# Kernel optimization log

Hardware: AMD Instinct MI355X
Metric: run time of the kernel (lower is better)

Reference implementation:

```python
import jax, jax.numpy as jnp
import numpy as np

D = 128  # embedding dimension (init arg d)

def setup_inputs() -> dict:
    key = jax.random.key(0)
    x = jax.random.uniform(key, (256, 4096), dtype=jnp.float32)  # (b, n) in [0,1]
    return {"x": x}

def reference(x) -> jnp.ndarray:
    # Fourier basis: emb[b, n, i] = cos(pi * i * x[b, n]), i = 0..D-1
    i = jnp.arange(D, dtype=x.dtype)  # (D,)
    emb = jnp.cos(jnp.pi * x[..., None] * i)  # (b, n, D)
    return emb
```

## Files before the change

### kernel.cpp

```cpp
#include <hip/hip_runtime.h>


typedef float f32x4 __attribute__((ext_vector_type(4)));

__global__ __launch_bounds__(256) void Emb_37967510896970_kernel(
    const float* __restrict__ x, f32x4* __restrict__ out, int total_rows)
{
    const int tid  = threadIdx.x;
    const int ty   = tid >> 5;
    const int slot = tid & 31;
    const int row0 = blockIdx.x * 64 + ty;

    float h[8];
#pragma unroll
    for (int q = 0; q < 8; ++q) {
        int r = row0 + 8 * q;
        h[q] = 0.5f * x[r < total_rows ? r : 0];
    }

    const float i0 = (float)(slot << 2);

    f32x4 v[8];
#pragma unroll
    for (int q = 0; q < 8; ++q) {
        const float hb = h[q] * i0;
#pragma unroll
        for (int k = 0; k < 4; ++k) {
            float ang = fmaf(h[q], (float)k, hb);
            v[q][k] = __builtin_amdgcn_cosf(__builtin_amdgcn_fractf(ang));
        }
    }

    f32x4* p = out + (size_t)blockIdx.x * 2048 + tid;
#pragma unroll
    for (int q = 0; q < 8; ++q) {
        int r = row0 + 8 * q;
        if (r < total_rows) __builtin_nontemporal_store(v[q], p + q * 256);
    }
}

extern "C" void kernel_launch(void* const* d_in, const int* in_sizes, int n_in,
                              void* d_out, int out_size, void* d_ws, size_t ws_size,
                              hipStream_t stream) {
    const float* x = (const float*)d_in[0];
    f32x4* out = (f32x4*)d_out;
    const int total_rows = in_sizes[0];
    const int grid = (total_rows + 63) / 64;
    Emb_37967510896970_kernel<<<grid, 256, 0, stream>>>(x, out, total_rows);
}
```

Baseline: 104.0 us.

## Use persistent grid-stride loop with prefetch of next rows' inputs

Replaces the one-block-per-64-rows launch with a fixed grid of 2048 blocks that loop over rows in grid strides. Each iteration prefetches the x values for the next stride before computing and storing the current one. The aim is to cut block scheduling overhead and hide the input load latency. In exchange, each thread carries extra registers, and a fixed grid may underfill or unbalance the device for other sizes.

```diff
diff --git a/kernel.cpp b/kernel.cpp
--- a/kernel.cpp
+++ b/kernel.cpp
@@ -9,33 +9,46 @@
     const int tid  = threadIdx.x;
     const int ty   = tid >> 5;
     const int slot = tid & 31;
-    const int row0 = blockIdx.x * 64 + ty;
+    const float i0 = (float)(slot << 2);
+    const int stride_rows = (int)gridDim.x * 64;
+
+    int base = blockIdx.x * 64;
 
     float h[8];
 #pragma unroll
     for (int q = 0; q < 8; ++q) {
-        int r = row0 + 8 * q;
+        int r = base + ty + 8 * q;
         h[q] = 0.5f * x[r < total_rows ? r : 0];
     }
 
-    const float i0 = (float)(slot << 2);
+    for (; base < total_rows; base += stride_rows) {
+        const int nb = base + stride_rows;
+        float hn[8];
+        if (nb < total_rows) {
+#pragma unroll
+            for (int q = 0; q < 8; ++q) {
+                int r = nb + ty + 8 * q;
+                hn[q] = 0.5f * x[r < total_rows ? r : 0];
+            }
+        }
 
-    f32x4 v[8];
+        f32x4* p = out + (size_t)base * 32 + tid;
 #pragma unroll
-    for (int q = 0; q < 8; ++q) {
-        const float hb = h[q] * i0;
+        for (int q = 0; q < 8; ++q) {
+            const float hq = h[q];
+            const float hb = hq * i0;
+            f32x4 v;
 #pragma unroll
-        for (int k = 0; k < 4; ++k) {
-            float ang = fmaf(h[q], (float)k, hb);
-            v[q][k] = __builtin_amdgcn_cosf(__builtin_amdgcn_fractf(ang));
+            for (int k = 0; k < 4; ++k)
+                v[k] = __builtin_amdgcn_cosf(
+                           __builtin_amdgcn_fractf(fmaf(hq, (float)k, hb)));
+            int r = base + ty + 8 * q;
+            if (r < total_rows)
+                __builtin_nontemporal_store(v, p + q * 256);
         }
-    }
 
-    f32x4* p = out + (size_t)blockIdx.x * 2048 + tid;
 #pragma unroll
-    for (int q = 0; q < 8; ++q) {
-        int r = row0 + 8 * q;
-        if (r < total_rows) __builtin_nontemporal_store(v[q], p + q * 256);
+        for (int q = 0; q < 8; ++q) h[q] = hn[q];
     }
 }
 
@@ -45,6 +58,6 @@
     const float* x = (const float*)d_in[0];
     f32x4* out = (f32x4*)d_out;
     const int total_rows = in_sizes[0];
-    const int grid = (total_rows + 63) / 64;
+    const int grid = 2048;
     Emb_37967510896970_kernel<<<grid, 256, 0, stream>>>(x, out, total_rows);
 }
```

After: 106.7 us. +2.6%, slower.

## Switch to persistent grid-stride kernel with prefetched input rows

Applied to the files above, without the earlier changes.

Replaces the one-block-per-64-rows launch with a fixed grid of 512 blocks that each sweep over rows with a grid stride. Each iteration computes and stores one 8-row by 128-column tile, and the x value two sweeps ahead is prefetched into a register rotation. The intent is to cut block launch overhead and keep stores streaming continuously. In exchange, each thread has less independent work in flight per iteration, and the persistent grid may underfill the GPU's compute units.

```diff
diff --git a/kernel.cpp b/kernel.cpp
--- a/kernel.cpp
+++ b/kernel.cpp
@@ -4,38 +4,41 @@
 typedef float f32x4 __attribute__((ext_vector_type(4)));
 
 __global__ __launch_bounds__(256) void Emb_37967510896970_kernel(
-    const float* __restrict__ x, f32x4* __restrict__ out, int total_rows)
+    const float* __restrict__ x, f32x4* __restrict__ out,
+    int total_rows, int nsweeps)
 {
     const int tid  = threadIdx.x;
     const int ty   = tid >> 5;
     const int slot = tid & 31;
-    const int row0 = blockIdx.x * 64 + ty;
-
-    float h[8];
-#pragma unroll
-    for (int q = 0; q < 8; ++q) {
-        int r = row0 + 8 * q;
-        h[q] = 0.5f * x[r < total_rows ? r : 0];
-    }
-
     const float i0 = (float)(slot << 2);
 
-    f32x4 v[8];
+    const int rstep = (int)gridDim.x * 8;
+    int row = blockIdx.x * 8 + ty;
+
+    float h0 = 0.5f * x[row < total_rows ? row : 0];
+    int r1 = row + rstep;
+    float h1 = 0.5f * x[r1 < total_rows ? r1 : 0];
+
+    f32x4* __restrict__ p = out + (size_t)blockIdx.x * 256 + tid;
+    const size_t pstep = (size_t)gridDim.x * 256;
+
+    for (int s = 0; s < nsweeps; ++s) {
+        int r2 = row + 2 * rstep;
+        float hn = 0.5f * x[r2 < total_rows ? r2 : 0];
+
+        const float hb = h0 * i0;
+        f32x4 v;
 #pragma unroll
-    for (int q = 0; q < 8; ++q) {
-        const float hb = h[q] * i0;
-#pragma unroll
-        for (int k = 0; k < 4; ++k) {
-            float ang = fmaf(h[q], (float)k, hb);
-            v[q][k] = __builtin_amdgcn_cosf(__builtin_amdgcn_fractf(ang));
-        }
-    }
+        for (int k = 0; k < 4; ++k)
+            v[k] = __builtin_amdgcn_cosf(
+                       __builtin_amdgcn_fractf(fmaf(h0, (float)k, hb)));
+        if (row < total_rows)
+            __builtin_nontemporal_store(v, p);
 
-    f32x4* p = out + (size_t)blockIdx.x * 2048 + tid;
-#pragma unroll
-    for (int q = 0; q < 8; ++q) {
-        int r = row0 + 8 * q;
-        if (r < total_rows) __builtin_nontemporal_store(v[q], p + q * 256);
+        p += pstep;
+        row += rstep;
+        h0 = h1;
+        h1 = hn;
     }
 }
 
@@ -45,6 +48,8 @@
     const float* x = (const float*)d_in[0];
     f32x4* out = (f32x4*)d_out;
     const int total_rows = in_sizes[0];
-    const int grid = (total_rows + 63) / 64;
-    Emb_37967510896970_kernel<<<grid, 256, 0, stream>>>(x, out, total_rows);
+    const int grid = 512;
+    const int rows_per_sweep = grid * 8;
+    const int nsweeps = (total_rows + rows_per_sweep - 1) / rows_per_sweep;
+    Emb_37967510896970_kernel<<<grid, 256, 0, stream>>>(x, out, total_rows, nsweeps);
 }
```

Result: no change. 102.7 us (-1.2%).

## Make each wave loop over many rows with x staged in shared memory

Applied to the files above, without the earlier changes.

Restructures the kernel so each block handles 4096 rows: x is loaded into LDS with vectorised loads, then each wave iterates over 1024 rows, two rows per iteration, with a software-pipelined prefetch of the next x value. This cuts the number of blocks and the redundant per-thread x loads. It trades away occupancy and memory-level parallelism, leaving one block of 4 waves per CU for a store-bound kernel.

```diff
diff --git a/kernel.cpp b/kernel.cpp
--- a/kernel.cpp
+++ b/kernel.cpp
@@ -3,39 +3,65 @@
 
 typedef float f32x4 __attribute__((ext_vector_type(4)));
 
+constexpr int ROWS_PER_WAVE  = 1024;
+constexpr int WAVES_PER_BLK  = 4;
+constexpr int ROWS_PER_BLK   = ROWS_PER_WAVE * WAVES_PER_BLK;
+
 __global__ __launch_bounds__(256) void Emb_37967510896970_kernel(
     const float* __restrict__ x, f32x4* __restrict__ out, int total_rows)
 {
-    const int tid  = threadIdx.x;
-    const int ty   = tid >> 5;
-    const int slot = tid & 31;
-    const int row0 = blockIdx.x * 64 + ty;
+    __shared__ float xs[ROWS_PER_BLK];
 
-    float h[8];
+    const int tid      = threadIdx.x;
+    const int blk_row0 = blockIdx.x * ROWS_PER_BLK;
+
+    {
+        const float4* xv = (const float4*)x + (blk_row0 >> 2);
+        float4*       sv = (float4*)xs;
 #pragma unroll
-    for (int q = 0; q < 8; ++q) {
-        int r = row0 + 8 * q;
-        h[q] = 0.5f * x[r < total_rows ? r : 0];
+        for (int j = 0; j < 4; ++j) {
+            int idx = j * 256 + tid;
+            int r   = blk_row0 + idx * 4;
+            float4 t = {0.f, 0.f, 0.f, 0.f};
+            if (r < total_rows) t = xv[idx];
+            sv[idx] = t;
+        }
     }
+    __syncthreads();
 
+    const int wave = tid >> 6;
+    const int lane = tid & 63;
+    const int slot = lane & 31;
+    const int rsel = lane >> 5;
     const float i0 = (float)(slot << 2);
 
-    f32x4 v[8];
+    const int    wrow0 = wave * ROWS_PER_WAVE;
+    const float* xw    = xs + wrow0;
+    f32x4*       p     = out + (size_t)(blk_row0 + wrow0) * 32 + lane;
+    int          grow  = blk_row0 + wrow0 + rsel;
+
+    constexpr int ITERS = ROWS_PER_WAVE / 2;
+
+    float hA = 0.5f * xw[0 + rsel];
+    float hB = 0.5f * xw[2 + rsel];
+
+#pragma unroll 4
+    for (int t = 0; t < ITERS; ++t) {
+        int   tn = t + 2;
+        float hC = 0.5f * xw[((tn < ITERS) ? 2 * tn : 0) + rsel];
+
+        const float hb = hA * i0;
+        f32x4 v;
 #pragma unroll
-    for (int q = 0; q < 8; ++q) {
-        const float hb = h[q] * i0;
-#pragma unroll
-        for (int k = 0; k < 4; ++k) {
-            float ang = fmaf(h[q], (float)k, hb);
-            v[q][k] = __builtin_amdgcn_cosf(__builtin_amdgcn_fractf(ang));
-        }
-    }
+        for (int k = 0; k < 4; ++k)
+            v[k] = __builtin_amdgcn_cosf(
+                       __builtin_amdgcn_fractf(fmaf(hA, (float)k, hb)));
+        if (grow < total_rows)
+            __builtin_nontemporal_store(v, p);
 
-    f32x4* p = out + (size_t)blockIdx.x * 2048 + tid;
-#pragma unroll
-    for (int q = 0; q < 8; ++q) {
-        int r = row0 + 8 * q;
-        if (r < total_rows) __builtin_nontemporal_store(v[q], p + q * 256);
+        p    += 64;
+        grow += 2;
+        hA = hB; hB = hC;
     }
 }
 
@@ -45,6 +71,6 @@
     const float* x = (const float*)d_in[0];
     f32x4* out = (f32x4*)d_out;
     const int total_rows = in_sizes[0];
-    const int grid = (total_rows + 63) / 64;
+    const int grid = (total_rows + ROWS_PER_BLK - 1) / ROWS_PER_BLK;
     Emb_37967510896970_kernel<<<grid, 256, 0, stream>>>(x, out, total_rows);
 }
```

Result: slower. 113.8 us (+9.4%).
